# Optimization experiments

Hardware: AMD Instinct MI355X
Metric: run time of the kernel (lower is better)

The kernel has to match this reference:

```python
import jax, jax.numpy as jnp
import numpy as np

B, N, M = 256, 512, 512


def setup_inputs() -> dict:
    key = jax.random.key(0)
    kx, kw, kt = jax.random.split(key, 3)
    x = jax.random.uniform(kx, (B, N), dtype=jnp.float32)
    w = jax.random.uniform(kw, (N, M), dtype=jnp.float32)
    t = jax.random.uniform(kt, (B, M), dtype=jnp.float32)
    return {"x": x, "w": w, "t": t}


def reference(x, w, t):
    # x: [B, N], w: [N, M], t: [B, M]
    x3 = x[:, :, None]   # [B, N, 1]
    t3 = t[:, None, :]   # [B, 1, M]
    w3 = w[None, :, :]   # [1, N, M]

    # relevance of x per (n, m): sum over batch of min(x, t) / sum over batch of x
    rel_x = jnp.minimum(x3, t3).sum(axis=0, keepdims=True) / x3.sum(axis=0, keepdims=True)  # [1, N, M]
    # relevance of w per (b, m): sum over N of min(w, t) / sum over N of w
    rel_w = jnp.minimum(w3, t3).sum(axis=-2, keepdims=True) / w3.sum(axis=-2, keepdims=True)  # [B, 1, M]

    # argmax over the N (inner) dimension
    ind_w = jnp.argmax(jnp.minimum(x3, rel_x), axis=-2)  # [B, M]
    ind_x = jnp.argmax(jnp.minimum(rel_w, w3), axis=-2)  # [B, M]

    # inner_x and inner_w are numerically identical in forward (detach only affects grads)
    inner = jnp.minimum(x3, w3)  # [B, N, M]
    chosen_x = jnp.take_along_axis(inner, ind_x[:, None, :], axis=-2)[:, 0, :]  # [B, M]
    chosen_w = jnp.take_along_axis(inner, ind_w[:, None, :], axis=-2)[:, 0, :]  # [B, M]
    return (chosen_x, chosen_w)
```

## Files before the change

kernel.cpp:

```cpp
#include <hip/hip_runtime.h>

#define B 256
#define N 512
#define M 512
#define BM (B * M)
#define NM (N * M)

__device__ __forceinline__ void tile_tr256(const float* __restrict__ src,
                                           float* __restrict__ dst,
                                           int R, int C, int r0, int c0, int tid) {
    __shared__ float s[64][65];
    const int tx = tid & 63, q = tid >> 6;
    #pragma unroll
    for (int j = 0; j < 16; ++j) {
        int rl = q * 16 + j;
        s[rl][tx] = src[(r0 + rl) * C + c0 + tx];
    }
    __syncthreads();
    #pragma unroll
    for (int j = 0; j < 16; ++j) {
        int cl = q * 16 + j;
        dst[(c0 + cl) * R + r0 + tx] = s[tx][cl];
    }
}

__global__ __launch_bounds__(256) void k_a(const float* __restrict__ x,
                                           const float* __restrict__ w,
                                           const float* __restrict__ t,
                                           float* __restrict__ xT,
                                           float* __restrict__ wT,
                                           float* __restrict__ tT,
                                           float* __restrict__ sum_x,
                                           float* __restrict__ sum_w,
                                           float* __restrict__ px) {
    const int blk = blockIdx.x, tid = threadIdx.x;
    if (blk < 32) {
        tile_tr256(x, xT, B, N, (blk >> 3) * 64, (blk & 7) * 64, tid);
    } else if (blk < 96) {
        int id = blk - 32;
        tile_tr256(w, wT, N, M, (id >> 3) * 64, (id & 7) * 64, tid);
    } else if (blk < 128) {
        int id = blk - 96;
        tile_tr256(t, tT, B, M, (id >> 3) * 64, (id & 7) * 64, tid);
    } else if (blk < 130) {
        const int i = (blk - 128) * 256 + tid;
        double a0 = 0, a1 = 0, a2 = 0, a3 = 0;
        for (int b = 0; b < B; b += 4) {
            a0 += (double)x[(b + 0) * N + i];
            a1 += (double)x[(b + 1) * N + i];
            a2 += (double)x[(b + 2) * N + i];
            a3 += (double)x[(b + 3) * N + i];
        }
        sum_x[i] = (float)((a0 + a1) + (a2 + a3));
    } else if (blk < 132) {
        const int mm = (blk - 130) * 256 + tid;
        double a0 = 0, a1 = 0, a2 = 0, a3 = 0;
        for (int n = 0; n < N; n += 4) {
            a0 += (double)w[(n + 0) * M + mm];
            a1 += (double)w[(n + 1) * M + mm];
            a2 += (double)w[(n + 2) * M + mm];
            a3 += (double)w[(n + 3) * M + mm];
        }
        sum_w[mm] = (float)((a0 + a1) + (a2 + a3));
    } else {
        const int rb  = blk - 132;
        const int z   = rb >> 7;
        const int rem = rb & 127;
        const int m0 = (rem & 7) * 64;
        const int n0 = (rem >> 3) * 32;
        const int tx = tid & 15, ty = tid >> 4;
        __shared__ float s_t[32][64];
        __shared__ float s_x[32][36];
        const int sr = tid >> 3, sc = tid & 7;
        float aA0 = 0.f, aA1 = 0.f, aA2 = 0.f, aA3 = 0.f;
        float aB0 = 0.f, aB1 = 0.f, aB2 = 0.f, aB3 = 0.f;
        const int nA = ty * 2, nB = nA + 1;
        for (int scnk = 0; scnk < 2; ++scnk) {
            const int bb = z * 64 + scnk * 32;
            __syncthreads();
            *(float4*)&s_t[sr][sc * 8]     = *(const float4*)&t[(bb + sr) * M + m0 + sc * 8];
            *(float4*)&s_t[sr][sc * 8 + 4] = *(const float4*)&t[(bb + sr) * M + m0 + sc * 8 + 4];
            *(float4*)&s_x[sr][sc * 4]     = *(const float4*)&x[(bb + sr) * N + n0 + sc * 4];
            __syncthreads();
            #pragma unroll 8
            for (int i = 0; i < 32; ++i) {
                float4 tv = *(const float4*)&s_t[i][tx * 4];
                float xA = s_x[i][nA], xB = s_x[i][nB];
                aA0 += fminf(xA, tv.x); aA1 += fminf(xA, tv.y);
                aA2 += fminf(xA, tv.z); aA3 += fminf(xA, tv.w);
                aB0 += fminf(xB, tv.x); aB1 += fminf(xB, tv.y);
                aB2 += fminf(xB, tv.z); aB3 += fminf(xB, tv.w);
            }
        }
        __syncthreads();
        float* so = &s_t[0][0];
        so[(tx * 4 + 0) * 32 + nA] = aA0; so[(tx * 4 + 0) * 32 + nB] = aB0;
        so[(tx * 4 + 1) * 32 + nA] = aA1; so[(tx * 4 + 1) * 32 + nB] = aB1;
        so[(tx * 4 + 2) * 32 + nA] = aA2; so[(tx * 4 + 2) * 32 + nB] = aB2;
        so[(tx * 4 + 3) * 32 + nA] = aA3; so[(tx * 4 + 3) * 32 + nB] = aB3;
        __syncthreads();
        const int m_l = tid >> 2, n_l = (tid & 3) * 8;
        float* dst = &px[z * NM + (m0 + m_l) * N + n0 + n_l];
        *(float4*)&dst[0] = *(const float4*)&so[m_l * 32 + n_l];
        *(float4*)&dst[4] = *(const float4*)&so[m_l * 32 + n_l + 4];
    }
}

__global__ __launch_bounds__(512) void k_col(
        const float* __restrict__ x, const float* __restrict__ xT,
        const float* __restrict__ wT, const float* __restrict__ tT,
        const float* __restrict__ px, const float* __restrict__ sum_x,
        const float* __restrict__ sum_w, float* __restrict__ out) {
    const int m = blockIdx.x, tid = threadIdx.x;
    const int lane = tid & 63, wid = tid >> 6;

    __shared__ float  worig[512], pm[512], wsrt[512];
    __shared__ float  srx_r[512], srx_u[512];
    __shared__ int    srx_n[512];
    __shared__ int    cnt[256], cbase[256], cslot[256];
    __shared__ int    rcnt[256], rbase[256], rslot[256], rbmax[256];
    __shared__ double bsumI[256];
    __shared__ float  wtotmax[8], red3[3][8];
    __shared__ int    ctot[4], rtot[4];
    __shared__ double btot[4];

    const float wv = wT[m * N + tid];
    float p = px[m * N + tid];
    p += px[NM + m * N + tid];
    p += px[2 * NM + m * N + tid];
    p += px[3 * NM + m * N + tid];
    const float rv = p / sum_x[tid];
    worig[tid] = wv;
    if (tid < 256) { cnt[tid] = 0; rcnt[tid] = 0; cslot[tid] = 0; rslot[tid] = 0; rbmax[tid] = 0; }

    float pmv = wv;
    #pragma unroll
    for (int off = 1; off < 64; off <<= 1) {
        float o = __shfl_up(pmv, off, 64);
        if (lane >= off) pmv = fmaxf(pmv, o);
    }
    if (lane == 63) wtotmax[wid] = pmv;
    float wmn = wv, rmn = rv, rmx = rv;
    #pragma unroll
    for (int off = 32; off > 0; off >>= 1) {
        wmn = fminf(wmn, __shfl_xor(wmn, off, 64));
        rmn = fminf(rmn, __shfl_xor(rmn, off, 64));
        rmx = fmaxf(rmx, __shfl_xor(rmx, off, 64));
    }
    if (lane == 0) { red3[0][wid] = wmn; red3[1][wid] = rmn; red3[2][wid] = rmx; }
    __syncthreads();

    {
        float om = -1e30f;
        for (int j = 0; j < wid; ++j) om = fmaxf(om, wtotmax[j]);
        pm[tid] = fmaxf(pmv, om);
    }
    float wmin = red3[0][0], rmin = red3[1][0], rmax = red3[2][0], wmax = wtotmax[0];
    #pragma unroll
    for (int j = 1; j < 8; ++j) {
        wmin = fminf(wmin, red3[0][j]);
        rmin = fminf(rmin, red3[1][j]);
        rmax = fmaxf(rmax, red3[2][j]);
        wmax = fmaxf(wmax, wtotmax[j]);
    }

    const float wscale = 255.0f / fmaxf(wmax - wmin, 1e-30f);
    int wk = (int)((wv - wmin) * wscale);
    wk = wk < 0 ? 0 : (wk > 255 ? 255 : wk);
    atomicAdd(&cnt[wk], 1);
    const float rscale = 255.0f / fmaxf(rmax - rmin, 1e-30f);
    int rk;
    { int kv = (int)((rv - rmin) * rscale); kv = kv < 0 ? 0 : (kv > 255 ? 255 : kv); rk = 255 - kv; }
    atomicAdd(&rcnt[rk], 1);
    atomicMax(&rbmax[rk], __float_as_int(rv));
    __syncthreads();

    int myc = (tid < 256) ? cnt[tid] : rcnt[tid - 256];
    int incl = myc;
    #pragma unroll
    for (int off = 1; off < 64; off <<= 1) {
        int o = __shfl_up(incl, off, 64);
        if (lane >= off) incl += o;
    }
    if (lane == 63) { if (wid < 4) ctot[wid] = incl; else rtot[wid - 4] = incl; }
    __syncthreads();
    if (tid < 256) {
        int eo = 0;
        for (int j = 0; j < wid; ++j) eo += ctot[j];
        cbase[tid] = eo + incl - myc;
    } else {
        int eo = 0, w2 = wid - 4;
        for (int j = 0; j < w2; ++j) eo += rtot[j];
        rbase[tid - 256] = eo + incl - myc;
    }
    __syncthreads();

    { int p1 = cbase[wk] + atomicAdd(&cslot[wk], 1); wsrt[p1] = wv; }
    { int p2 = rbase[rk] + atomicAdd(&rslot[rk], 1);
      srx_r[p2] = rv; srx_n[p2] = tid; srx_u[p2] = __int_as_float(rbmax[rk]); }
    __syncthreads();

    double bincl = 0.0, mysum = 0.0;
    if (tid < 256) {
        int st = cbase[tid], e = st + cnt[tid];
        for (int i = st; i < e; ++i) mysum += (double)wsrt[i];
        bincl = mysum;
        #pragma unroll
        for (int off = 1; off < 64; off <<= 1) {
            double o = __shfl_up(bincl, off, 64);
            if (lane >= off) bincl += o;
        }
        if (lane == 63) btot[wid] = bincl;
    }
    __syncthreads();
    if (tid < 256) {
        double eo = 0.0;
        for (int j = 0; j < wid; ++j) eo += btot[j];
        bsumI[tid] = eo + bincl;
    }
    __syncthreads();

    if (tid < 256) {
        const int b = tid;
        float bv = -1.0f; int bi = 0;
        for (int i = 0; i < 512; ++i) {
            float u = srx_u[i];
            if (__ballot(u >= bv) == 0ULL) break;
            float r = srx_r[i];
            int   n = srx_n[i];
            float xv = xT[n * B + b];
            float v = fminf(xv, r);
            if (v > bv || (v == bv && n < bi)) { bv = v; bi = n; }
        }
        out[BM + b * M + m] = fminf(x[b * N + bi], worig[bi]);
    } else {
        const int b = tid - 256;
        const float tbm = tT[m * B + b];
        float btf = (tbm - wmin) * wscale;
        int kk; double S;
        if (btf < 0.0f) { kk = 0; S = 0.0; }
        else {
            int bt = (int)btf; bt = bt > 255 ? 255 : bt;
            kk = cbase[bt];
            S = (bt > 0) ? bsumI[bt - 1] : 0.0;
            int e = cbase[bt] + cnt[bt];
            for (int i = cbase[bt]; i < e; ++i) {
                float v = wsrt[i];
                if (v < tbm) { ++kk; S += (double)v; }
            }
        }
        double rw = S + (double)tbm * (double)(512 - kk);
        float c = (float)rw / sum_w[m];
        float tgt = fminf(c, pm[511]);
        int lo = 0, hi = 511;
        while (lo < hi) { int mid = (lo + hi) >> 1; if (pm[mid] >= tgt) hi = mid; else lo = mid + 1; }
        const int ind = lo;
        out[b * M + m] = fminf(x[b * N + ind], worig[ind]);
    }
}

extern "C" void kernel_launch(void* const* d_in, const int* in_sizes, int n_in,
                              void* d_out, int out_size, void* d_ws, size_t ws_size,
                              hipStream_t stream) {
    const float* x = (const float*)d_in[0];
    const float* w = (const float*)d_in[1];
    const float* t = (const float*)d_in[2];
    float* out = (float*)d_out;

    float* ws = (float*)d_ws;
    float* xT    = ws;
    float* wT    = ws + 131072;
    float* tT    = ws + 393216;
    float* sum_x = ws + 524288;
    float* sum_w = ws + 524800;
    float* px    = ws + 525312;

    k_a  <<<644, 256, 0, stream>>>(x, w, t, xT, wT, tT, sum_x, sum_w, px);
    k_col<<<512, 512, 0, stream>>>(x, xT, wT, tT, px, sum_x, sum_w, out);
}
```

Before: 89.54 us.

## Fuse both kernels into one persistent kernel with a grid-wide atomic barrier

Merges the transpose/partial-sum kernel and the per-column selection kernel into a single 256-block, 512-thread launch. A global atomic counter, reset by a memset, acts as a grid barrier between the phases, and each block handles two partial-product tiles and two output columns. This removes one kernel launch and the gap between kernels, at the cost of a spin barrier that requires all 256 blocks to be co-resident. It also adds a memset call and leaves fewer blocks doing the column phase.

```diff
diff --git a/kernel.cpp b/kernel.cpp
--- a/kernel.cpp
+++ b/kernel.cpp
@@ -6,114 +6,37 @@
 #define BM (B * M)
 #define NM (N * M)
 
-__device__ __forceinline__ void tile_tr256(const float* __restrict__ src,
+
+__device__ __forceinline__ void tile_tr512(const float* __restrict__ src,
                                            float* __restrict__ dst,
                                            int R, int C, int r0, int c0, int tid) {
     __shared__ float s[64][65];
     const int tx = tid & 63, q = tid >> 6;
     #pragma unroll
-    for (int j = 0; j < 16; ++j) {
-        int rl = q * 16 + j;
+    for (int j = 0; j < 8; ++j) {
+        int rl = q * 8 + j;
         s[rl][tx] = src[(r0 + rl) * C + c0 + tx];
     }
     __syncthreads();
     #pragma unroll
-    for (int j = 0; j < 16; ++j) {
-        int cl = q * 16 + j;
+    for (int j = 0; j < 8; ++j) {
+        int cl = q * 8 + j;
         dst[(c0 + cl) * R + r0 + tx] = s[tx][cl];
     }
 }
 
-__global__ __launch_bounds__(256) void k_a(const float* __restrict__ x,
-                                           const float* __restrict__ w,
-                                           const float* __restrict__ t,
-                                           float* __restrict__ xT,
-                                           float* __restrict__ wT,
-                                           float* __restrict__ tT,
-                                           float* __restrict__ sum_x,
-                                           float* __restrict__ sum_w,
-                                           float* __restrict__ px) {
+__global__ __launch_bounds__(512) void k_fused(
+        const float* __restrict__ x, const float* __restrict__ w,
+        const float* __restrict__ t, float* __restrict__ xT,
+        float* __restrict__ wT, float* __restrict__ tT,
+        float* __restrict__ sum_x, float* __restrict__ sum_w,
+        float* __restrict__ px, int* __restrict__ bar,
+        float* __restrict__ out) {
     const int blk = blockIdx.x, tid = threadIdx.x;
-    if (blk < 32) {
-        tile_tr256(x, xT, B, N, (blk >> 3) * 64, (blk & 7) * 64, tid);
-    } else if (blk < 96) {
-        int id = blk - 32;
-        tile_tr256(w, wT, N, M, (id >> 3) * 64, (id & 7) * 64, tid);
-    } else if (blk < 128) {
-        int id = blk - 96;
-        tile_tr256(t, tT, B, M, (id >> 3) * 64, (id & 7) * 64, tid);
-    } else if (blk < 130) {
-        const int i = (blk - 128) * 256 + tid;
-        double a0 = 0, a1 = 0, a2 = 0, a3 = 0;
-        for (int b = 0; b < B; b += 4) {
-            a0 += (double)x[(b + 0) * N + i];
-            a1 += (double)x[(b + 1) * N + i];
-            a2 += (double)x[(b + 2) * N + i];
-            a3 += (double)x[(b + 3) * N + i];
-        }
-        sum_x[i] = (float)((a0 + a1) + (a2 + a3));
-    } else if (blk < 132) {
-        const int mm = (blk - 130) * 256 + tid;
-        double a0 = 0, a1 = 0, a2 = 0, a3 = 0;
-        for (int n = 0; n < N; n += 4) {
-            a0 += (double)w[(n + 0) * M + mm];
-            a1 += (double)w[(n + 1) * M + mm];
-            a2 += (double)w[(n + 2) * M + mm];
-            a3 += (double)w[(n + 3) * M + mm];
-        }
-        sum_w[mm] = (float)((a0 + a1) + (a2 + a3));
-    } else {
-        const int rb  = blk - 132;
-        const int z   = rb >> 7;
-        const int rem = rb & 127;
-        const int m0 = (rem & 7) * 64;
-        const int n0 = (rem >> 3) * 32;
-        const int tx = tid & 15, ty = tid >> 4;
-        __shared__ float s_t[32][64];
-        __shared__ float s_x[32][36];
-        const int sr = tid >> 3, sc = tid & 7;
-        float aA0 = 0.f, aA1 = 0.f, aA2 = 0.f, aA3 = 0.f;
-        float aB0 = 0.f, aB1 = 0.f, aB2 = 0.f, aB3 = 0.f;
-        const int nA = ty * 2, nB = nA + 1;
-        for (int scnk = 0; scnk < 2; ++scnk) {
-            const int bb = z * 64 + scnk * 32;
-            __syncthreads();
-            *(float4*)&s_t[sr][sc * 8]     = *(const float4*)&t[(bb + sr) * M + m0 + sc * 8];
-            *(float4*)&s_t[sr][sc * 8 + 4] = *(const float4*)&t[(bb + sr) * M + m0 + sc * 8 + 4];
-            *(float4*)&s_x[sr][sc * 4]     = *(const float4*)&x[(bb + sr) * N + n0 + sc * 4];
-            __syncthreads();
-            #pragma unroll 8
-            for (int i = 0; i < 32; ++i) {
-                float4 tv = *(const float4*)&s_t[i][tx * 4];
-                float xA = s_x[i][nA], xB = s_x[i][nB];
-                aA0 += fminf(xA, tv.x); aA1 += fminf(xA, tv.y);
-                aA2 += fminf(xA, tv.z); aA3 += fminf(xA, tv.w);
-                aB0 += fminf(xB, tv.x); aB1 += fminf(xB, tv.y);
-                aB2 += fminf(xB, tv.z); aB3 += fminf(xB, tv.w);
-            }
-        }
-        __syncthreads();
-        float* so = &s_t[0][0];
-        so[(tx * 4 + 0) * 32 + nA] = aA0; so[(tx * 4 + 0) * 32 + nB] = aB0;
-        so[(tx * 4 + 1) * 32 + nA] = aA1; so[(tx * 4 + 1) * 32 + nB] = aB1;
-        so[(tx * 4 + 2) * 32 + nA] = aA2; so[(tx * 4 + 2) * 32 + nB] = aB2;
-        so[(tx * 4 + 3) * 32 + nA] = aA3; so[(tx * 4 + 3) * 32 + nB] = aB3;
-        __syncthreads();
-        const int m_l = tid >> 2, n_l = (tid & 3) * 8;
-        float* dst = &px[z * NM + (m0 + m_l) * N + n0 + n_l];
-        *(float4*)&dst[0] = *(const float4*)&so[m_l * 32 + n_l];
-        *(float4*)&dst[4] = *(const float4*)&so[m_l * 32 + n_l + 4];
-    }
-}
-
-__global__ __launch_bounds__(512) void k_col(
-        const float* __restrict__ x, const float* __restrict__ xT,
-        const float* __restrict__ wT, const float* __restrict__ tT,
-        const float* __restrict__ px, const float* __restrict__ sum_x,
-        const float* __restrict__ sum_w, float* __restrict__ out) {
-    const int m = blockIdx.x, tid = threadIdx.x;
     const int lane = tid & 63, wid = tid >> 6;
 
+    __shared__ float s_t[32][64];
+    __shared__ float s_x[32][36];
     __shared__ float  worig[512], pm[512], wsrt[512];
     __shared__ float  srx_r[512], srx_u[512];
     __shared__ int    srx_n[512];
@@ -124,138 +47,222 @@
     __shared__ int    ctot[4], rtot[4];
     __shared__ double btot[4];
 
-    const float wv = wT[m * N + tid];
-    float p = px[m * N + tid];
-    p += px[NM + m * N + tid];
-    p += px[2 * NM + m * N + tid];
-    p += px[3 * NM + m * N + tid];
-    const float rv = p / sum_x[tid];
-    worig[tid] = wv;
-    if (tid < 256) { cnt[tid] = 0; rcnt[tid] = 0; cslot[tid] = 0; rslot[tid] = 0; rbmax[tid] = 0; }
-
-    float pmv = wv;
-    #pragma unroll
-    for (int off = 1; off < 64; off <<= 1) {
-        float o = __shfl_up(pmv, off, 64);
-        if (lane >= off) pmv = fmaxf(pmv, o);
-    }
-    if (lane == 63) wtotmax[wid] = pmv;
-    float wmn = wv, rmn = rv, rmx = rv;
-    #pragma unroll
-    for (int off = 32; off > 0; off >>= 1) {
-        wmn = fminf(wmn, __shfl_xor(wmn, off, 64));
-        rmn = fminf(rmn, __shfl_xor(rmn, off, 64));
-        rmx = fmaxf(rmx, __shfl_xor(rmx, off, 64));
-    }
-    if (lane == 0) { red3[0][wid] = wmn; red3[1][wid] = rmn; red3[2][wid] = rmx; }
+    if (blk < 32) {
+        tile_tr512(x, xT, B, N, (blk >> 3) * 64, (blk & 7) * 64, tid);
+    } else if (blk < 96) {
+        int id = blk - 32;
+        tile_tr512(w, wT, N, M, (id >> 3) * 64, (id & 7) * 64, tid);
+    } else if (blk < 128) {
+        int id = blk - 96;
+        tile_tr512(t, tT, B, M, (id >> 3) * 64, (id & 7) * 64, tid);
+    } else if (blk == 128) {
+        const int i = tid;
+        double a0 = 0, a1 = 0, a2 = 0, a3 = 0;
+        for (int b = 0; b < B; b += 4) {
+            a0 += (double)x[(b + 0) * N + i];
+            a1 += (double)x[(b + 1) * N + i];
+            a2 += (double)x[(b + 2) * N + i];
+            a3 += (double)x[(b + 3) * N + i];
+        }
+        sum_x[i] = (float)((a0 + a1) + (a2 + a3));
+    } else if (blk == 129) {
+        const int mm = tid;
+        double a0 = 0, a1 = 0, a2 = 0, a3 = 0;
+        for (int n = 0; n < N; n += 4) {
+            a0 += (double)w[(n + 0) * M + mm];
+            a1 += (double)w[(n + 1) * M + mm];
+            a2 += (double)w[(n + 2) * M + mm];
+            a3 += (double)w[(n + 3) * M + mm];
+        }
+        sum_w[mm] = (float)((a0 + a1) + (a2 + a3));
+    }
+
+    const int tx = tid & 15;
+    const int ny = tid >> 4;
+    #pragma unroll 1
+    for (int r = 0; r < 2; ++r) {
+        const int id = blk * 2 + r;
+        const int z   = id >> 7;
+        const int rem = id & 127;
+        const int m0 = (rem & 7) * 64;
+        const int n0 = (rem >> 3) * 32;
+        float a0 = 0.f, a1 = 0.f, a2 = 0.f, a3 = 0.f;
+        for (int scnk = 0; scnk < 2; ++scnk) {
+            const int bb = z * 64 + scnk * 32;
+            __syncthreads();
+            { int sr = tid >> 4, sc = (tid & 15) * 4;
+              *(float4*)&s_t[sr][sc] = *(const float4*)&t[(bb + sr) * M + m0 + sc]; }
+            if (tid < 256) {
+                int sr2 = tid >> 3, sc2 = (tid & 7) * 4;
+                *(float4*)&s_x[sr2][sc2] = *(const float4*)&x[(bb + sr2) * N + n0 + sc2];
+            }
+            __syncthreads();
+            #pragma unroll 8
+            for (int i = 0; i < 32; ++i) {
+                float4 tv = *(const float4*)&s_t[i][tx * 4];
+                float xv = s_x[i][ny];
+                a0 += fminf(xv, tv.x); a1 += fminf(xv, tv.y);
+                a2 += fminf(xv, tv.z); a3 += fminf(xv, tv.w);
+            }
+        }
+        __syncthreads();
+        float* so = &s_t[0][0];
+        so[(tx * 4 + 0) * 32 + ny] = a0;
+        so[(tx * 4 + 1) * 32 + ny] = a1;
+        so[(tx * 4 + 2) * 32 + ny] = a2;
+        so[(tx * 4 + 3) * 32 + ny] = a3;
+        __syncthreads();
+        const int m_l = tid >> 3, n_l4 = (tid & 7) * 4;
+        *(float4*)&px[z * NM + (m0 + m_l) * N + n0 + n_l4] =
+            *(const float4*)&so[m_l * 32 + n_l4];
+    }
+
     __syncthreads();
-
-    {
-        float om = -1e30f;
-        for (int j = 0; j < wid; ++j) om = fmaxf(om, wtotmax[j]);
-        pm[tid] = fmaxf(pmv, om);
-    }
-    float wmin = red3[0][0], rmin = red3[1][0], rmax = red3[2][0], wmax = wtotmax[0];
-    #pragma unroll
-    for (int j = 1; j < 8; ++j) {
-        wmin = fminf(wmin, red3[0][j]);
-        rmin = fminf(rmin, red3[1][j]);
-        rmax = fmaxf(rmax, red3[2][j]);
-        wmax = fmaxf(wmax, wtotmax[j]);
-    }
-
-    const float wscale = 255.0f / fmaxf(wmax - wmin, 1e-30f);
-    int wk = (int)((wv - wmin) * wscale);
-    wk = wk < 0 ? 0 : (wk > 255 ? 255 : wk);
-    atomicAdd(&cnt[wk], 1);
-    const float rscale = 255.0f / fmaxf(rmax - rmin, 1e-30f);
-    int rk;
-    { int kv = (int)((rv - rmin) * rscale); kv = kv < 0 ? 0 : (kv > 255 ? 255 : kv); rk = 255 - kv; }
-    atomicAdd(&rcnt[rk], 1);
-    atomicMax(&rbmax[rk], __float_as_int(rv));
+    if (tid == 0) {
+        __threadfence();
+        atomicAdd(bar, 1);
+        while (__hip_atomic_load(bar, __ATOMIC_RELAXED, __HIP_MEMORY_SCOPE_AGENT) < 256) { }
+    }
     __syncthreads();
-
-    int myc = (tid < 256) ? cnt[tid] : rcnt[tid - 256];
-    int incl = myc;
-    #pragma unroll
-    for (int off = 1; off < 64; off <<= 1) {
-        int o = __shfl_up(incl, off, 64);
-        if (lane >= off) incl += o;
-    }
-    if (lane == 63) { if (wid < 4) ctot[wid] = incl; else rtot[wid - 4] = incl; }
-    __syncthreads();
-    if (tid < 256) {
-        int eo = 0;
-        for (int j = 0; j < wid; ++j) eo += ctot[j];
-        cbase[tid] = eo + incl - myc;
-    } else {
-        int eo = 0, w2 = wid - 4;
-        for (int j = 0; j < w2; ++j) eo += rtot[j];
-        rbase[tid - 256] = eo + incl - myc;
-    }
-    __syncthreads();
-
-    { int p1 = cbase[wk] + atomicAdd(&cslot[wk], 1); wsrt[p1] = wv; }
-    { int p2 = rbase[rk] + atomicAdd(&rslot[rk], 1);
-      srx_r[p2] = rv; srx_n[p2] = tid; srx_u[p2] = __int_as_float(rbmax[rk]); }
-    __syncthreads();
-
-    double bincl = 0.0, mysum = 0.0;
-    if (tid < 256) {
-        int st = cbase[tid], e = st + cnt[tid];
-        for (int i = st; i < e; ++i) mysum += (double)wsrt[i];
-        bincl = mysum;
+    __threadfence();
+
+    for (int mi = 0; mi < 2; ++mi) {
+        const int m = blk * 2 + mi;
+        __syncthreads();
+
+        const float wv = wT[m * N + tid];
+        float p = px[m * N + tid];
+        p += px[NM + m * N + tid];
+        p += px[2 * NM + m * N + tid];
+        p += px[3 * NM + m * N + tid];
+        const float rv = p / sum_x[tid];
+        worig[tid] = wv;
+        if (tid < 256) { cnt[tid] = 0; rcnt[tid] = 0; cslot[tid] = 0; rslot[tid] = 0; rbmax[tid] = 0; }
+
+        float pmv = wv;
         #pragma unroll
         for (int off = 1; off < 64; off <<= 1) {
-            double o = __shfl_up(bincl, off, 64);
-            if (lane >= off) bincl += o;
-        }
-        if (lane == 63) btot[wid] = bincl;
-    }
-    __syncthreads();
-    if (tid < 256) {
-        double eo = 0.0;
-        for (int j = 0; j < wid; ++j) eo += btot[j];
-        bsumI[tid] = eo + bincl;
-    }
-    __syncthreads();
-
-    if (tid < 256) {
-        const int b = tid;
-        float bv = -1.0f; int bi = 0;
-        for (int i = 0; i < 512; ++i) {
-            float u = srx_u[i];
-            if (__ballot(u >= bv) == 0ULL) break;
-            float r = srx_r[i];
-            int   n = srx_n[i];
-            float xv = xT[n * B + b];
-            float v = fminf(xv, r);
-            if (v > bv || (v == bv && n < bi)) { bv = v; bi = n; }
-        }
-        out[BM + b * M + m] = fminf(x[b * N + bi], worig[bi]);
-    } else {
-        const int b = tid - 256;
-        const float tbm = tT[m * B + b];
-        float btf = (tbm - wmin) * wscale;
-        int kk; double S;
-        if (btf < 0.0f) { kk = 0; S = 0.0; }
-        else {
-            int bt = (int)btf; bt = bt > 255 ? 255 : bt;
-            kk = cbase[bt];
-            S = (bt > 0) ? bsumI[bt - 1] : 0.0;
-            int e = cbase[bt] + cnt[bt];
-            for (int i = cbase[bt]; i < e; ++i) {
-                float v = wsrt[i];
-                if (v < tbm) { ++kk; S += (double)v; }
-            }
-        }
-        double rw = S + (double)tbm * (double)(512 - kk);
-        float c = (float)rw / sum_w[m];
-        float tgt = fminf(c, pm[511]);
-        int lo = 0, hi = 511;
-        while (lo < hi) { int mid = (lo + hi) >> 1; if (pm[mid] >= tgt) hi = mid; else lo = mid + 1; }
-        const int ind = lo;
-        out[b * M + m] = fminf(x[b * N + ind], worig[ind]);
+            float o = __shfl_up(pmv, off, 64);
+            if (lane >= off) pmv = fmaxf(pmv, o);
+        }
+        if (lane == 63) wtotmax[wid] = pmv;
+        float wmn = wv, rmn = rv, rmx = rv;
+        #pragma unroll
+        for (int off = 32; off > 0; off >>= 1) {
+            wmn = fminf(wmn, __shfl_xor(wmn, off, 64));
+            rmn = fminf(rmn, __shfl_xor(rmn, off, 64));
+            rmx = fmaxf(rmx, __shfl_xor(rmx, off, 64));
+        }
+        if (lane == 0) { red3[0][wid] = wmn; red3[1][wid] = rmn; red3[2][wid] = rmx; }
+        __syncthreads();
+
+        {
+            float om = -1e30f;
+            for (int j = 0; j < wid; ++j) om = fmaxf(om, wtotmax[j]);
+            pm[tid] = fmaxf(pmv, om);
+        }
+        float wmin = red3[0][0], rmin = red3[1][0], rmax = red3[2][0], wmax = wtotmax[0];
+        #pragma unroll
+        for (int j = 1; j < 8; ++j) {
+            wmin = fminf(wmin, red3[0][j]);
+            rmin = fminf(rmin, red3[1][j]);
+            rmax = fmaxf(rmax, red3[2][j]);
+            wmax = fmaxf(wmax, wtotmax[j]);
+        }
+
+        const float wscale = 255.0f / fmaxf(wmax - wmin, 1e-30f);
+        int wk = (int)((wv - wmin) * wscale);
+        wk = wk < 0 ? 0 : (wk > 255 ? 255 : wk);
+        atomicAdd(&cnt[wk], 1);
+        const float rscale = 255.0f / fmaxf(rmax - rmin, 1e-30f);
+        int rk;
+        { int kv = (int)((rv - rmin) * rscale); kv = kv < 0 ? 0 : (kv > 255 ? 255 : kv); rk = 255 - kv; }
+        atomicAdd(&rcnt[rk], 1);
+        atomicMax(&rbmax[rk], __float_as_int(rv));
+        __syncthreads();
+
+        int myc = (tid < 256) ? cnt[tid] : rcnt[tid - 256];
+        int incl = myc;
+        #pragma unroll
+        for (int off = 1; off < 64; off <<= 1) {
+            int o = __shfl_up(incl, off, 64);
+            if (lane >= off) incl += o;
+        }
+        if (lane == 63) { if (wid < 4) ctot[wid] = incl; else rtot[wid - 4] = incl; }
+        __syncthreads();
+        if (tid < 256) {
+            int eo = 0;
+            for (int j = 0; j < wid; ++j) eo += ctot[j];
+            cbase[tid] = eo + incl - myc;
+        } else {
+            int eo = 0, w2 = wid - 4;
+            for (int j = 0; j < w2; ++j) eo += rtot[j];
+            rbase[tid - 256] = eo + incl - myc;
+        }
+        __syncthreads();
+
+        { int p1 = cbase[wk] + atomicAdd(&cslot[wk], 1); wsrt[p1] = wv; }
+        { int p2 = rbase[rk] + atomicAdd(&rslot[rk], 1);
+          srx_r[p2] = rv; srx_n[p2] = tid; srx_u[p2] = __int_as_float(rbmax[rk]); }
+        __syncthreads();
+
+        double bincl = 0.0, mysum = 0.0;
+        if (tid < 256) {
+            int st = cbase[tid], e = st + cnt[tid];
+            for (int i = st; i < e; ++i) mysum += (double)wsrt[i];
+            bincl = mysum;
+            #pragma unroll
+            for (int off = 1; off < 64; off <<= 1) {
+                double o = __shfl_up(bincl, off, 64);
+                if (lane >= off) bincl += o;
+            }
+            if (lane == 63) btot[wid] = bincl;
+        }
+        __syncthreads();
+        if (tid < 256) {
+            double eo = 0.0;
+            for (int j = 0; j < wid; ++j) eo += btot[j];
+            bsumI[tid] = eo + bincl;
+        }
+        __syncthreads();
+
+        if (tid < 256) {
+            const int b = tid;
+            float bv = -1.0f; int bi = 0;
+            for (int i = 0; i < 512; ++i) {
+                float u = srx_u[i];
+                if (__ballot(u >= bv) == 0ULL) break;
+                float r = srx_r[i];
+                int   n = srx_n[i];
+                float xv = xT[n * B + b];
+                float v = fminf(xv, r);
+                if (v > bv || (v == bv && n < bi)) { bv = v; bi = n; }
+            }
+            out[BM + b * M + m] = fminf(x[b * N + bi], worig[bi]);
+        } else {
+            const int b = tid - 256;
+            const float tbm = tT[m * B + b];
+            float btf = (tbm - wmin) * wscale;
+            int kk; double S;
+            if (btf < 0.0f) { kk = 0; S = 0.0; }
+            else {
+                int bt = (int)btf; bt = bt > 255 ? 255 : bt;
+                kk = cbase[bt];
+                S = (bt > 0) ? bsumI[bt - 1] : 0.0;
+                int e = cbase[bt] + cnt[bt];
+                for (int i = cbase[bt]; i < e; ++i) {
+                    float v = wsrt[i];
+                    if (v < tbm) { ++kk; S += (double)v; }
+                }
+            }
+            double rw = S + (double)tbm * (double)(512 - kk);
+            float c = (float)rw / sum_w[m];
+            float tgt = fminf(c, pm[511]);
+            int lo = 0, hi = 511;
+            while (lo < hi) { int mid = (lo + hi) >> 1; if (pm[mid] >= tgt) hi = mid; else lo = mid + 1; }
+            const int ind = lo;
+            out[b * M + m] = fminf(x[b * N + ind], worig[ind]);
+        }
     }
 }
 
@@ -274,7 +281,8 @@
     float* sum_x = ws + 524288;
     float* sum_w = ws + 524800;
     float* px    = ws + 525312;
-
-    k_a  <<<644, 256, 0, stream>>>(x, w, t, xT, wT, tT, sum_x, sum_w, px);
-    k_col<<<512, 512, 0, stream>>>(x, xT, wT, tT, px, sum_x, sum_w, out);
+    int*   bar   = (int*)(ws + 1573888);
+
+    hipMemsetAsync(bar, 0, sizeof(int), stream);
+    k_fused<<<256, 512, 0, stream>>>(x, w, t, xT, wT, tT, sum_x, sum_w, px, bar, out);
 }
```

New measurement: 150.4 us. +68.0%, slower.

## Fuse rel_x partial sums into column kernel, removing px intermediate buffer

Applied to the files above, without the earlier changes.

Computes the per-column sum of min(x,t) and sum of x inside the column kernel, reading x and a shared-memory copy of the t column directly. This drops the separate partial-sum stage in the first kernel and the large px workspace round trip, and shrinks the first kernel's grid. The cost is that each column block redundantly reads all of x and recomputes sum_x with double-precision accumulation in a serial loop.

```diff
diff --git a/kernel.cpp b/kernel.cpp
--- a/kernel.cpp
+++ b/kernel.cpp
@@ -4,7 +4,6 @@
 #define N 512
 #define M 512
 #define BM (B * M)
-#define NM (N * M)
 
 __device__ __forceinline__ void tile_tr256(const float* __restrict__ src,
                                            float* __restrict__ dst,
@@ -30,9 +29,7 @@
                                            float* __restrict__ xT,
                                            float* __restrict__ wT,
                                            float* __restrict__ tT,
-                                           float* __restrict__ sum_x,
-                                           float* __restrict__ sum_w,
-                                           float* __restrict__ px) {
+                                           float* __restrict__ sum_w) {
     const int blk = blockIdx.x, tid = threadIdx.x;
     if (blk < 32) {
         tile_tr256(x, xT, B, N, (blk >> 3) * 64, (blk & 7) * 64, tid);
@@ -42,78 +39,28 @@
     } else if (blk < 128) {
         int id = blk - 96;
         tile_tr256(t, tT, B, M, (id >> 3) * 64, (id & 7) * 64, tid);
-    } else if (blk < 130) {
-        const int i = (blk - 128) * 256 + tid;
-        double a0 = 0, a1 = 0, a2 = 0, a3 = 0;
-        for (int b = 0; b < B; b += 4) {
-            a0 += (double)x[(b + 0) * N + i];
-            a1 += (double)x[(b + 1) * N + i];
-            a2 += (double)x[(b + 2) * N + i];
-            a3 += (double)x[(b + 3) * N + i];
-        }
-        sum_x[i] = (float)((a0 + a1) + (a2 + a3));
-    } else if (blk < 132) {
-        const int mm = (blk - 130) * 256 + tid;
-        double a0 = 0, a1 = 0, a2 = 0, a3 = 0;
-        for (int n = 0; n < N; n += 4) {
-            a0 += (double)w[(n + 0) * M + mm];
-            a1 += (double)w[(n + 1) * M + mm];
-            a2 += (double)w[(n + 2) * M + mm];
-            a3 += (double)w[(n + 3) * M + mm];
-        }
-        sum_w[mm] = (float)((a0 + a1) + (a2 + a3));
     } else {
-        const int rb  = blk - 132;
-        const int z   = rb >> 7;
-        const int rem = rb & 127;
-        const int m0 = (rem & 7) * 64;
-        const int n0 = (rem >> 3) * 32;
-        const int tx = tid & 15, ty = tid >> 4;
-        __shared__ float s_t[32][64];
-        __shared__ float s_x[32][36];
-        const int sr = tid >> 3, sc = tid & 7;
-        float aA0 = 0.f, aA1 = 0.f, aA2 = 0.f, aA3 = 0.f;
-        float aB0 = 0.f, aB1 = 0.f, aB2 = 0.f, aB3 = 0.f;
-        const int nA = ty * 2, nB = nA + 1;
-        for (int scnk = 0; scnk < 2; ++scnk) {
-            const int bb = z * 64 + scnk * 32;
-            __syncthreads();
-            *(float4*)&s_t[sr][sc * 8]     = *(const float4*)&t[(bb + sr) * M + m0 + sc * 8];
-            *(float4*)&s_t[sr][sc * 8 + 4] = *(const float4*)&t[(bb + sr) * M + m0 + sc * 8 + 4];
-            *(float4*)&s_x[sr][sc * 4]     = *(const float4*)&x[(bb + sr) * N + n0 + sc * 4];
-            __syncthreads();
-            #pragma unroll 8
-            for (int i = 0; i < 32; ++i) {
-                float4 tv = *(const float4*)&s_t[i][tx * 4];
-                float xA = s_x[i][nA], xB = s_x[i][nB];
-                aA0 += fminf(xA, tv.x); aA1 += fminf(xA, tv.y);
-                aA2 += fminf(xA, tv.z); aA3 += fminf(xA, tv.w);
-                aB0 += fminf(xB, tv.x); aB1 += fminf(xB, tv.y);
-                aB2 += fminf(xB, tv.z); aB3 += fminf(xB, tv.w);
+        for (int mm = tid; mm < M; mm += 256) {
+            double a0 = 0, a1 = 0, a2 = 0, a3 = 0;
+            for (int n = 0; n < N; n += 4) {
+                a0 += (double)w[(n + 0) * M + mm];
+                a1 += (double)w[(n + 1) * M + mm];
+                a2 += (double)w[(n + 2) * M + mm];
+                a3 += (double)w[(n + 3) * M + mm];
             }
-        }
-        __syncthreads();
-        float* so = &s_t[0][0];
-        so[(tx * 4 + 0) * 32 + nA] = aA0; so[(tx * 4 + 0) * 32 + nB] = aB0;
-        so[(tx * 4 + 1) * 32 + nA] = aA1; so[(tx * 4 + 1) * 32 + nB] = aB1;
-        so[(tx * 4 + 2) * 32 + nA] = aA2; so[(tx * 4 + 2) * 32 + nB] = aB2;
-        so[(tx * 4 + 3) * 32 + nA] = aA3; so[(tx * 4 + 3) * 32 + nB] = aB3;
-        __syncthreads();
-        const int m_l = tid >> 2, n_l = (tid & 3) * 8;
-        float* dst = &px[z * NM + (m0 + m_l) * N + n0 + n_l];
-        *(float4*)&dst[0] = *(const float4*)&so[m_l * 32 + n_l];
-        *(float4*)&dst[4] = *(const float4*)&so[m_l * 32 + n_l + 4];
+            sum_w[mm] = (float)((a0 + a1) + (a2 + a3));
+        }
     }
 }
 
 __global__ __launch_bounds__(512) void k_col(
         const float* __restrict__ x, const float* __restrict__ xT,
         const float* __restrict__ wT, const float* __restrict__ tT,
-        const float* __restrict__ px, const float* __restrict__ sum_x,
         const float* __restrict__ sum_w, float* __restrict__ out) {
     const int m = blockIdx.x, tid = threadIdx.x;
     const int lane = tid & 63, wid = tid >> 6;
 
+    __shared__ float  tcol[256];
     __shared__ float  worig[512], pm[512], wsrt[512];
     __shared__ float  srx_r[512], srx_u[512];
     __shared__ int    srx_n[512];
@@ -124,14 +71,34 @@
     __shared__ int    ctot[4], rtot[4];
     __shared__ double btot[4];
 
+    if (tid < 256) tcol[tid] = tT[m * B + tid];
+    if (tid < 256) { cnt[tid] = 0; rcnt[tid] = 0; cslot[tid] = 0; rslot[tid] = 0; rbmax[tid] = 0; }
+    __syncthreads();
+
+    const float* xc = x + tid;
+    float q0 = 0.f, q1 = 0.f, q2 = 0.f, q3 = 0.f;
+    double a0 = 0, a1 = 0, a2 = 0, a3 = 0;
+    #pragma unroll 1
+    for (int z = 0; z < 4; ++z) {
+        float s = 0.f;
+        #pragma unroll 4
+        for (int b4 = z * 64; b4 < z * 64 + 64; b4 += 4) {
+            float x0 = xc[(b4 + 0) * N], t0 = tcol[b4 + 0];
+            float x1 = xc[(b4 + 1) * N], t1 = tcol[b4 + 1];
+            float x2 = xc[(b4 + 2) * N], t2 = tcol[b4 + 2];
+            float x3 = xc[(b4 + 3) * N], t3 = tcol[b4 + 3];
+            s += fminf(x0, t0); s += fminf(x1, t1);
+            s += fminf(x2, t2); s += fminf(x3, t3);
+            a0 += (double)x0; a1 += (double)x1;
+            a2 += (double)x2; a3 += (double)x3;
+        }
+        if (z == 0) q0 = s; else if (z == 1) q1 = s; else if (z == 2) q2 = s; else q3 = s;
+    }
+    const float p = ((q0 + q1) + q2) + q3;
+    const float sxf = (float)((a0 + a1) + (a2 + a3));
+    const float rv = p / sxf;
     const float wv = wT[m * N + tid];
-    float p = px[m * N + tid];
-    p += px[NM + m * N + tid];
-    p += px[2 * NM + m * N + tid];
-    p += px[3 * NM + m * N + tid];
-    const float rv = p / sum_x[tid];
     worig[tid] = wv;
-    if (tid < 256) { cnt[tid] = 0; rcnt[tid] = 0; cslot[tid] = 0; rslot[tid] = 0; rbmax[tid] = 0; }
 
     float pmv = wv;
     #pragma unroll
@@ -235,7 +202,7 @@
         out[BM + b * M + m] = fminf(x[b * N + bi], worig[bi]);
     } else {
         const int b = tid - 256;
-        const float tbm = tT[m * B + b];
+        const float tbm = tcol[b];
         float btf = (tbm - wmin) * wscale;
         int kk; double S;
         if (btf < 0.0f) { kk = 0; S = 0.0; }
@@ -271,10 +238,8 @@
     float* xT    = ws;
     float* wT    = ws + 131072;
     float* tT    = ws + 393216;
-    float* sum_x = ws + 524288;
-    float* sum_w = ws + 524800;
-    float* px    = ws + 525312;
-
-    k_a  <<<644, 256, 0, stream>>>(x, w, t, xT, wT, tT, sum_x, sum_w, px);
-    k_col<<<512, 512, 0, stream>>>(x, xT, wT, tT, px, sum_x, sum_w, out);
-}
+    float* sum_w = ws + 524288;
+
+    k_a  <<<129, 256, 0, stream>>>(x, w, t, xT, wT, tT, sum_w);
+    k_col<<<512, 512, 0, stream>>>(x, xT, wT, tT, sum_w, out);
+}
```

Result: slower. 115.4 us (+28.9%).
